# Performance work log

Measured on AMD Instinct MI355X. Metric: run time of the kernel, lower is better.

The kernel has to match this reference:

```python
import jax, jax.numpy as jnp
import numpy as np

B, S = 4096, 256
D = 32  # output_size // 4


def setup_inputs() -> dict:
    key = jax.random.key(0)
    ks = jax.random.split(key, 32)
    # continuous features
    cont_p = jax.random.normal(ks[0], (B, S, 3), dtype=jnp.float32)
    cont_c = jax.random.normal(ks[1], (B, S, 2), dtype=jnp.float32)
    # categorical features, per-column vocab sizes from Embedding tables
    vocabs_p = [2, 2, 2, 11, 34]
    cat_p = jnp.stack([
        jax.random.randint(ks[2 + i], (B, S), 0, v, dtype=jnp.int32)
        for i, v in enumerate(vocabs_p)], axis=2)
    vocabs_c = [19, 31]
    cat_c = jnp.stack([
        jax.random.randint(ks[7 + i], (B, S), 0, v, dtype=jnp.int32)
        for i, v in enumerate(vocabs_c)], axis=2)
    lengths = jax.random.randint(ks[9], (B,), 1, S + 1, dtype=jnp.int32)

    def lin(k, fan_in, fan_out):
        bound = 1.0 / np.sqrt(fan_in)
        kw, kb = jax.random.split(k)
        w = jax.random.uniform(kw, (fan_in, fan_out), jnp.float32, -bound, bound)
        b = jax.random.uniform(kb, (fan_out,), jnp.float32, -bound, bound)
        return w, b

    w_p1, b_p1 = lin(ks[10], 3, D)
    w_p2, b_p2 = lin(ks[11], D, D)
    w_c1, b_c1 = lin(ks[12], 2, D)
    w_c2, b_c2 = lin(ks[13], D, D)
    emb_gender = jax.random.normal(ks[14], (2, D), dtype=jnp.float32)
    emb_korean = jax.random.normal(ks[15], (2, D), dtype=jnp.float32)
    emb_primary = jax.random.normal(ks[16], (2, D), dtype=jnp.float32)
    emb_job = jax.random.normal(ks[17], (11, D), dtype=jnp.float32)
    emb_rep = jax.random.normal(ks[18], (34, D), dtype=jnp.float32)
    emb_place = jax.random.normal(ks[19], (19, D), dtype=jnp.float32)
    emb_add = jax.random.normal(ks[20], (31, D), dtype=jnp.float32)
    w_fc1, b_fc1 = lin(ks[21], 128, 64)
    w_fc2, b_fc2 = lin(ks[22], 64, 2)

    return dict(cont_p=cont_p, cont_c=cont_c, cat_p=cat_p, cat_c=cat_c,
                lengths=lengths,
                w_p1=w_p1, b_p1=b_p1, w_p2=w_p2, b_p2=b_p2,
                w_c1=w_c1, b_c1=b_c1, w_c2=w_c2, b_c2=b_c2,
                emb_gender=emb_gender, emb_korean=emb_korean,
                emb_primary=emb_primary, emb_job=emb_job, emb_rep=emb_rep,
                emb_place=emb_place, emb_add=emb_add,
                w_fc1=w_fc1, b_fc1=b_fc1, w_fc2=w_fc2, b_fc2=b_fc2)


def reference(cont_p, cont_c, cat_p, cat_c, lengths,
              w_p1, b_p1, w_p2, b_p2, w_c1, b_c1, w_c2, b_c2,
              emb_gender, emb_korean, emb_primary, emb_job, emb_rep,
              emb_place, emb_add, w_fc1, b_fc1, w_fc2, b_fc2):
    # small per-token MLPs on continuous features -> [B,S,D]
    hp = jax.nn.relu(cont_p @ w_p1 + b_p1) @ w_p2 + b_p2
    hc = jax.nn.relu(cont_c @ w_c1 + b_c1) @ w_c2 + b_c2
    # multi-table embedding lookups, averaged per group -> [B,S,D]
    ep = (emb_gender[cat_p[:, :, 0]] + emb_korean[cat_p[:, :, 1]] +
          emb_primary[cat_p[:, :, 2]] + emb_job[cat_p[:, :, 3]] +
          emb_rep[cat_p[:, :, 4]]) / 5.0
    ec = (emb_place[cat_c[:, :, 0]] + emb_add[cat_c[:, :, 1]]) / 2.0
    # concat order matches torch: (cat_p, cat_c, cont_p, cont_c) -> [B,S,128]
    x = jnp.concatenate([ep, ec, hp, hc], axis=2)
    # ragged mean pool over first lengths[i] positions (masked segment mean)
    mask = (jnp.arange(x.shape[1])[None, :] < lengths[:, None])
    pooled = jnp.sum(x * mask[:, :, None], axis=1) / lengths[:, None].astype(x.dtype)
    # head: relu(fc1) -> relu(fc2); dropout p=0.0 is identity
    h = jax.nn.relu(pooled @ w_fc1 + b_fc1)
    return jax.nn.relu(h @ w_fc2 + b_fc2)
```

## Files before the change

### kernel.cpp

```cpp
#include <hip/hip_runtime.h>


#define BDIM 64

__device__ __forceinline__ float wave_sum64(float v) {
    #pragma unroll
    for (int d = 32; d; d >>= 1) v += __shfl_xor(v, d);
    return v;
}

__device__ __forceinline__ float transpose_reduce32(const float a[32], int lane) {
    float x16[16];
    {
        const bool s = (lane & 16) != 0;
        #pragma unroll
        for (int i = 0; i < 16; ++i) {
            float keep = s ? a[16 + i] : a[i];
            float send = s ? a[i] : a[16 + i];
            x16[i] = keep + __shfl_xor(send, 16);
        }
    }
    float x8[8];
    {
        const bool s = (lane & 8) != 0;
        #pragma unroll
        for (int i = 0; i < 8; ++i) {
            float keep = s ? x16[8 + i] : x16[i];
            float send = s ? x16[i] : x16[8 + i];
            x8[i] = keep + __shfl_xor(send, 8);
        }
    }
    float x4[4];
    {
        const bool s = (lane & 4) != 0;
        #pragma unroll
        for (int i = 0; i < 4; ++i) {
            float keep = s ? x8[4 + i] : x8[i];
            float send = s ? x8[i] : x8[4 + i];
            x4[i] = keep + __shfl_xor(send, 4);
        }
    }
    float x2[2];
    {
        const bool s = (lane & 2) != 0;
        #pragma unroll
        for (int i = 0; i < 2; ++i) {
            float keep = s ? x2[0] * 0.f + x4[2 + i] : x4[i];
            (void)keep;
            float k2 = s ? x4[2 + i] : x4[i];
            float send = s ? x4[i] : x4[2 + i];
            x2[i] = k2 + __shfl_xor(send, 2);
        }
    }
    float v;
    {
        const bool s = (lane & 1) != 0;
        float keep = s ? x2[1] : x2[0];
        float send = s ? x2[0] : x2[1];
        v = keep + __shfl_xor(send, 1);
    }
    v += __shfl_xor(v, 32);
    return v;
}

__global__ __launch_bounds__(BDIM, 4)
void mlpreg_kernel(const float* __restrict__ cont_p,
                   const float* __restrict__ cont_c,
                   const int* __restrict__ cat_p,
                   const int* __restrict__ cat_c,
                   const int* __restrict__ lengths,
                   const float* __restrict__ w_p1, const float* __restrict__ b_p1,
                   const float* __restrict__ w_p2, const float* __restrict__ b_p2,
                   const float* __restrict__ w_c1, const float* __restrict__ b_c1,
                   const float* __restrict__ w_c2, const float* __restrict__ b_c2,
                   const float* __restrict__ emb_g,  const float* __restrict__ emb_k,
                   const float* __restrict__ emb_pr, const float* __restrict__ emb_j,
                   const float* __restrict__ emb_r,  const float* __restrict__ emb_pl,
                   const float* __restrict__ emb_a,
                   const float* __restrict__ w_fc1, const float* __restrict__ b_fc1,
                   const float* __restrict__ w_fc2, const float* __restrict__ b_fc2,
                   float* __restrict__ out)
{
    constexpr int S = 256;
    __shared__ int   hist[96];
    __shared__ float sPacc[64];
    __shared__ __align__(16) float sPool[128];

    const int lane = threadIdx.x;
    const int b    = blockIdx.x;
    int L = lengths[b];
    L = (L < 1) ? 1 : (L > S ? S : L);
    const float Lf = (float)L, invL = 1.0f / Lf;

    hist[lane] = 0;
    if (lane < 32) hist[64 + lane] = 0;

    const int ch = lane & 31, h = lane >> 5;
    const float* gp = cont_p + (size_t)b * (S * 3);
    const float* gc = cont_c + (size_t)b * (S * 2);
    const int*   kp = cat_p  + (size_t)b * (S * 5);
    const int*   kc = cat_c  + (size_t)b * (S * 2);

    const int t0 = lane, t1 = 64 + lane;
    const int i0 = (t0 < L) ? t0 : (L - 1);
    const int i1 = (t1 < L) ? t1 : (L - 1);
    const float m0 = (t0 < L) ? 1.f : 0.f;
    const float m1 = (t1 < L) ? 1.f : 0.f;
    float a00 = gp[3 * i0], a01 = gp[3 * i0 + 1], a02 = gp[3 * i0 + 2];
    float2 e0 = *(const float2*)&gc[2 * i0];
    float a10 = gp[3 * i1], a11 = gp[3 * i1 + 1], a12 = gp[3 * i1 + 2];
    float2 e1 = *(const float2*)&gc[2 * i1];

    int pk = 0;
    #pragma unroll
    for (int blk = 0; blk < 4; ++blk) {
        if (L > blk * 64) {
            int t = blk * 64 + lane;
            if (t < L) {
                int v0 = kp[5 * t], v1 = kp[5 * t + 1], v2 = kp[5 * t + 2],
                    v3 = kp[5 * t + 3], v4 = kp[5 * t + 4];
                int2 q = *(const int2*)&kc[2 * t];
                pk += v0 + (v1 << 10) + (v2 << 20);
                atomicAdd(&hist[v3], 1);
                atomicAdd(&hist[11 + v4], 1);
                atomicAdd(&hist[46 + q.x], 1);
                atomicAdd(&hist[65 + q.y], 1);
            }
        }
    }
    #pragma unroll
    for (int d = 32; d; d >>= 1) pk += __shfl_xor(pk, d);
    const float sg = (float)(pk & 1023), sk = (float)((pk >> 10) & 1023),
                sp = (float)(pk >> 20);

    float AP[32], AC[32];
    #pragma unroll
    for (int j = 0; j < 32; ++j) {
        float vp = fmaf(a00, w_p1[j], fmaf(a01, w_p1[32 + j], fmaf(a02, w_p1[64 + j], b_p1[j])));
        AP[j] = m0 * fmaxf(vp, 0.f);
        float vc = fmaf(e0.x, w_c1[j], fmaf(e0.y, w_c1[32 + j], b_c1[j]));
        AC[j] = m0 * fmaxf(vc, 0.f);
    }
    if (L > 64) {
        #pragma unroll
        for (int j = 0; j < 32; ++j) {
            float vp = fmaf(a10, w_p1[j], fmaf(a11, w_p1[32 + j], fmaf(a12, w_p1[64 + j], b_p1[j])));
            AP[j] = fmaf(m1, fmaxf(vp, 0.f), AP[j]);
            float vc = fmaf(e1.x, w_c1[j], fmaf(e1.y, w_c1[32 + j], b_c1[j]));
            AC[j] = fmaf(m1, fmaxf(vc, 0.f), AC[j]);
        }
    }
    if (L > 128) {
        int t = 128 + lane;
        int ti = (t < L) ? t : (L - 1);
        float m = (t < L) ? 1.f : 0.f;
        float c0 = gp[3 * ti], c1 = gp[3 * ti + 1], c2 = gp[3 * ti + 2];
        float2 dd = *(const float2*)&gc[2 * ti];
        #pragma unroll
        for (int j = 0; j < 32; ++j) {
            float vp = fmaf(c0, w_p1[j], fmaf(c1, w_p1[32 + j], fmaf(c2, w_p1[64 + j], b_p1[j])));
            AP[j] = fmaf(m, fmaxf(vp, 0.f), AP[j]);
            float vc = fmaf(dd.x, w_c1[j], fmaf(dd.y, w_c1[32 + j], b_c1[j]));
            AC[j] = fmaf(m, fmaxf(vc, 0.f), AC[j]);
        }
    }
    if (L > 192) {
        int t = 192 + lane;
        int ti = (t < L) ? t : (L - 1);
        float m = (t < L) ? 1.f : 0.f;
        float c0 = gp[3 * ti], c1 = gp[3 * ti + 1], c2 = gp[3 * ti + 2];
        float2 dd = *(const float2*)&gc[2 * ti];
        #pragma unroll
        for (int j = 0; j < 32; ++j) {
            float vp = fmaf(c0, w_p1[j], fmaf(c1, w_p1[32 + j], fmaf(c2, w_p1[64 + j], b_p1[j])));
            AP[j] = fmaf(m, fmaxf(vp, 0.f), AP[j]);
            float vc = fmaf(dd.x, w_c1[j], fmaf(dd.y, w_c1[32 + j], b_c1[j]));
            AC[j] = fmaf(m, fmaxf(vc, 0.f), AC[j]);
        }
    }

    float paccP = transpose_reduce32(AP, lane);
    float paccC = transpose_reduce32(AC, lane);
    if (lane < 32) {
        sPacc[ch]      = paccP * invL;
        sPacc[32 + ch] = paccC * invL;
    }
    __syncthreads();

    float vp0 = h ? 0.f : b_p2[ch];
    #pragma unroll
    for (int i = 0; i < 16; ++i) {
        int k = h * 16 + i;
        vp0 = fmaf(sPacc[k], w_p2[k * 32 + ch], vp0);
    }
    vp0 += __shfl_down(vp0, 32);
    float vc0 = h ? 0.f : b_c2[ch];
    #pragma unroll
    for (int i = 0; i < 16; ++i) {
        int k = h * 16 + i;
        vc0 = fmaf(sPacc[32 + k], w_c2[k * 32 + ch], vc0);
    }
    vc0 += __shfl_down(vc0, 32);

    float ep = 0.f;
    if (h == 0) {
        ep  = fmaf(Lf - sg, emb_g[ch],  sg * emb_g[32 + ch]);
        ep += fmaf(Lf - sk, emb_k[ch],  sk * emb_k[32 + ch]);
        ep += fmaf(Lf - sp, emb_pr[ch], sp * emb_pr[32 + ch]);
    }
    #pragma unroll
    for (int i = 0; i < 23; ++i) {
        int bb = 2 * i + h;
        int cnt = hist[bb];
        int br = (bb < 44) ? bb : 44;
        const float* tp = (bb < 11) ? (emb_j + bb * 32) : (emb_r + (br - 11) * 32);
        ep = fmaf((float)cnt, tp[ch], ep);
    }
    ep += __shfl_down(ep, 32);
    float ec = 0.f;
    #pragma unroll
    for (int i = 0; i < 25; ++i) {
        int bb = 46 + 2 * i + h;
        int cnt = hist[bb];
        const float* tp = (bb < 65) ? (emb_pl + (bb - 46) * 32) : (emb_a + (bb - 65) * 32);
        ec = fmaf((float)cnt, tp[ch], ec);
    }
    ec += __shfl_down(ec, 32);

    if (lane < 32) {
        sPool[ch]      = ep * (invL * 0.2f);
        sPool[32 + ch] = ec * (invL * 0.5f);
        sPool[64 + ch] = vp0;
        sPool[96 + ch] = vc0;
    }
    __syncthreads();

    float q0 = b_fc1[lane], q1 = 0.f, q2 = 0.f, q3 = 0.f;
    #pragma unroll
    for (int k4 = 0; k4 < 32; ++k4) {
        float4 x = *(const float4*)&sPool[4 * k4];
        q0 = fmaf(x.x, w_fc1[(size_t)(4 * k4 + 0) * 64 + lane], q0);
        q1 = fmaf(x.y, w_fc1[(size_t)(4 * k4 + 1) * 64 + lane], q1);
        q2 = fmaf(x.z, w_fc1[(size_t)(4 * k4 + 2) * 64 + lane], q2);
        q3 = fmaf(x.w, w_fc1[(size_t)(4 * k4 + 3) * 64 + lane], q3);
    }
    float hv = fmaxf((q0 + q1) + (q2 + q3), 0.f);

    float2 wf = *(const float2*)&w_fc2[2 * lane];
    float p0 = wave_sum64(hv * wf.x);
    float p1 = wave_sum64(hv * wf.y);
    if (lane == 0) {
        float2 o2;
        o2.x = fmaxf(p0 + b_fc2[0], 0.f);
        o2.y = fmaxf(p1 + b_fc2[1], 0.f);
        *(float2*)&out[(size_t)b * 2] = o2;
    }
}

extern "C" void kernel_launch(void* const* d_in, const int* in_sizes, int n_in,
                              void* d_out, int out_size, void* d_ws, size_t ws_size,
                              hipStream_t stream) {
    const float* cont_p = (const float*)d_in[0];
    const float* cont_c = (const float*)d_in[1];
    const int*   cat_p  = (const int*)d_in[2];
    const int*   cat_c  = (const int*)d_in[3];
    const int*   lens   = (const int*)d_in[4];
    const float* w_p1   = (const float*)d_in[5];
    const float* b_p1   = (const float*)d_in[6];
    const float* w_p2   = (const float*)d_in[7];
    const float* b_p2   = (const float*)d_in[8];
    const float* w_c1   = (const float*)d_in[9];
    const float* b_c1   = (const float*)d_in[10];
    const float* w_c2   = (const float*)d_in[11];
    const float* b_c2   = (const float*)d_in[12];
    const float* emb_g  = (const float*)d_in[13];
    const float* emb_k  = (const float*)d_in[14];
    const float* emb_pr = (const float*)d_in[15];
    const float* emb_j  = (const float*)d_in[16];
    const float* emb_r  = (const float*)d_in[17];
    const float* emb_pl = (const float*)d_in[18];
    const float* emb_a  = (const float*)d_in[19];
    const float* w_fc1  = (const float*)d_in[20];
    const float* b_fc1  = (const float*)d_in[21];
    const float* w_fc2  = (const float*)d_in[22];
    const float* b_fc2  = (const float*)d_in[23];
    float* out = (float*)d_out;

    hipLaunchKernelGGL(mlpreg_kernel, dim3(4096), dim3(BDIM), 0, stream,
                       cont_p, cont_c, cat_p, cat_c, lens,
                       w_p1, b_p1, w_p2, b_p2, w_c1, b_c1, w_c2, b_c2,
                       emb_g, emb_k, emb_pr, emb_j, emb_r, emb_pl, emb_a,
                       w_fc1, b_fc1, w_fc2, b_fc2, out);
}
```

Baseline: 162.4 us.

## Stage token features in LDS and loop over tokens with per-lane output channels

Continuous token features are first copied with coalesced loads into a padded shared-memory tile. Each lane then owns one hidden channel (P or C branch) and loops over all valid tokens, reading them as LDS broadcasts. This replaces the per-lane 32-wide register arrays and the transpose-reduce shuffle tree. Work now scales with L and removes the register pressure, but it adds a serial loop of up to 256 iterations per lane and an extra barrier.

```diff
diff --git a/kernel.cpp b/kernel.cpp
--- a/kernel.cpp
+++ b/kernel.cpp
@@ -6,60 +6,6 @@
 __device__ __forceinline__ float wave_sum64(float v) {
     #pragma unroll
     for (int d = 32; d; d >>= 1) v += __shfl_xor(v, d);
-    return v;
-}
-
-__device__ __forceinline__ float transpose_reduce32(const float a[32], int lane) {
-    float x16[16];
-    {
-        const bool s = (lane & 16) != 0;
-        #pragma unroll
-        for (int i = 0; i < 16; ++i) {
-            float keep = s ? a[16 + i] : a[i];
-            float send = s ? a[i] : a[16 + i];
-            x16[i] = keep + __shfl_xor(send, 16);
-        }
-    }
-    float x8[8];
-    {
-        const bool s = (lane & 8) != 0;
-        #pragma unroll
-        for (int i = 0; i < 8; ++i) {
-            float keep = s ? x16[8 + i] : x16[i];
-            float send = s ? x16[i] : x16[8 + i];
-            x8[i] = keep + __shfl_xor(send, 8);
-        }
-    }
-    float x4[4];
-    {
-        const bool s = (lane & 4) != 0;
-        #pragma unroll
-        for (int i = 0; i < 4; ++i) {
-            float keep = s ? x8[4 + i] : x8[i];
-            float send = s ? x8[i] : x8[4 + i];
-            x4[i] = keep + __shfl_xor(send, 4);
-        }
-    }
-    float x2[2];
-    {
-        const bool s = (lane & 2) != 0;
-        #pragma unroll
-        for (int i = 0; i < 2; ++i) {
-            float keep = s ? x2[0] * 0.f + x4[2 + i] : x4[i];
-            (void)keep;
-            float k2 = s ? x4[2 + i] : x4[i];
-            float send = s ? x4[i] : x4[2 + i];
-            x2[i] = k2 + __shfl_xor(send, 2);
-        }
-    }
-    float v;
-    {
-        const bool s = (lane & 1) != 0;
-        float keep = s ? x2[1] : x2[0];
-        float send = s ? x2[0] : x2[1];
-        v = keep + __shfl_xor(send, 1);
-    }
-    v += __shfl_xor(v, 32);
     return v;
 }
 
@@ -82,6 +28,7 @@
                    float* __restrict__ out)
 {
     constexpr int S = 256;
+    __shared__ __align__(16) float sTok[S * 8];
     __shared__ int   hist[96];
     __shared__ float sPacc[64];
     __shared__ __align__(16) float sPool[128];
@@ -101,15 +48,19 @@
     const int*   kp = cat_p  + (size_t)b * (S * 5);
     const int*   kc = cat_c  + (size_t)b * (S * 2);
 
-    const int t0 = lane, t1 = 64 + lane;
-    const int i0 = (t0 < L) ? t0 : (L - 1);
-    const int i1 = (t1 < L) ? t1 : (L - 1);
-    const float m0 = (t0 < L) ? 1.f : 0.f;
-    const float m1 = (t1 < L) ? 1.f : 0.f;
-    float a00 = gp[3 * i0], a01 = gp[3 * i0 + 1], a02 = gp[3 * i0 + 2];
-    float2 e0 = *(const float2*)&gc[2 * i0];
-    float a10 = gp[3 * i1], a11 = gp[3 * i1 + 1], a12 = gp[3 * i1 + 2];
-    float2 e1 = *(const float2*)&gc[2 * i1];
+    const float w0 = h ? w_c1[ch]      : w_p1[ch];
+    const float w1 = h ? w_c1[32 + ch] : w_p1[32 + ch];
+    const float w2 = h ? 0.f           : w_p1[64 + ch];
+    const float bb = h ? b_c1[ch]      : b_p1[ch];
+
+    for (int i = lane; i < 3 * L; i += BDIM) {
+        int t = i / 3, r = i - 3 * t;
+        sTok[t * 8 + r] = gp[i];
+    }
+    for (int i = lane; i < 2 * L; i += BDIM) {
+        int t = i >> 1, r = i & 1;
+        sTok[t * 8 + 4 + r] = gc[i];
+    }
 
     int pk = 0;
     #pragma unroll
@@ -133,58 +84,22 @@
     const float sg = (float)(pk & 1023), sk = (float)((pk >> 10) & 1023),
                 sp = (float)(pk >> 20);
 
-    float AP[32], AC[32];
-    #pragma unroll
-    for (int j = 0; j < 32; ++j) {
-        float vp = fmaf(a00, w_p1[j], fmaf(a01, w_p1[32 + j], fmaf(a02, w_p1[64 + j], b_p1[j])));
-        AP[j] = m0 * fmaxf(vp, 0.f);
-        float vc = fmaf(e0.x, w_c1[j], fmaf(e0.y, w_c1[32 + j], b_c1[j]));
-        AC[j] = m0 * fmaxf(vc, 0.f);
-    }
-    if (L > 64) {
-        #pragma unroll
-        for (int j = 0; j < 32; ++j) {
-            float vp = fmaf(a10, w_p1[j], fmaf(a11, w_p1[32 + j], fmaf(a12, w_p1[64 + j], b_p1[j])));
-            AP[j] = fmaf(m1, fmaxf(vp, 0.f), AP[j]);
-            float vc = fmaf(e1.x, w_c1[j], fmaf(e1.y, w_c1[32 + j], b_c1[j]));
-            AC[j] = fmaf(m1, fmaxf(vc, 0.f), AC[j]);
-        }
-    }
-    if (L > 128) {
-        int t = 128 + lane;
-        int ti = (t < L) ? t : (L - 1);
-        float m = (t < L) ? 1.f : 0.f;
-        float c0 = gp[3 * ti], c1 = gp[3 * ti + 1], c2 = gp[3 * ti + 2];
-        float2 dd = *(const float2*)&gc[2 * ti];
-        #pragma unroll
-        for (int j = 0; j < 32; ++j) {
-            float vp = fmaf(c0, w_p1[j], fmaf(c1, w_p1[32 + j], fmaf(c2, w_p1[64 + j], b_p1[j])));
-            AP[j] = fmaf(m, fmaxf(vp, 0.f), AP[j]);
-            float vc = fmaf(dd.x, w_c1[j], fmaf(dd.y, w_c1[32 + j], b_c1[j]));
-            AC[j] = fmaf(m, fmaxf(vc, 0.f), AC[j]);
-        }
-    }
-    if (L > 192) {
-        int t = 192 + lane;
-        int ti = (t < L) ? t : (L - 1);
-        float m = (t < L) ? 1.f : 0.f;
-        float c0 = gp[3 * ti], c1 = gp[3 * ti + 1], c2 = gp[3 * ti + 2];
-        float2 dd = *(const float2*)&gc[2 * ti];
-        #pragma unroll
-        for (int j = 0; j < 32; ++j) {
-            float vp = fmaf(c0, w_p1[j], fmaf(c1, w_p1[32 + j], fmaf(c2, w_p1[64 + j], b_p1[j])));
-            AP[j] = fmaf(m, fmaxf(vp, 0.f), AP[j]);
-            float vc = fmaf(dd.x, w_c1[j], fmaf(dd.y, w_c1[32 + j], b_c1[j]));
-            AC[j] = fmaf(m, fmaxf(vc, 0.f), AC[j]);
-        }
-    }
-
-    float paccP = transpose_reduce32(AP, lane);
-    float paccC = transpose_reduce32(AC, lane);
-    if (lane < 32) {
-        sPacc[ch]      = paccP * invL;
-        sPacc[32 + ch] = paccC * invL;
-    }
+    __syncthreads();
+
+    const int off = h << 2;
+    float acc0 = 0.f, acc1 = 0.f;
+    int t = 0;
+    for (; t + 1 < L; t += 2) {
+        float4 va = *(const float4*)&sTok[t * 8 + off];
+        float4 vb = *(const float4*)&sTok[(t + 1) * 8 + off];
+        acc0 += fmaxf(fmaf(va.x, w0, fmaf(va.y, w1, fmaf(va.z, w2, bb))), 0.f);
+        acc1 += fmaxf(fmaf(vb.x, w0, fmaf(vb.y, w1, fmaf(vb.z, w2, bb))), 0.f);
+    }
+    if (t < L) {
+        float4 va = *(const float4*)&sTok[t * 8 + off];
+        acc0 += fmaxf(fmaf(va.x, w0, fmaf(va.y, w1, fmaf(va.z, w2, bb))), 0.f);
+    }
+    sPacc[lane] = (acc0 + acc1) * invL;
     __syncthreads();
 
     float vp0 = h ? 0.f : b_p2[ch];
@@ -210,19 +125,19 @@
     }
     #pragma unroll
     for (int i = 0; i < 23; ++i) {
-        int bb = 2 * i + h;
-        int cnt = hist[bb];
-        int br = (bb < 44) ? bb : 44;
-        const float* tp = (bb < 11) ? (emb_j + bb * 32) : (emb_r + (br - 11) * 32);
+        int bb2 = 2 * i + h;
+        int cnt = hist[bb2];
+        int br = (bb2 < 44) ? bb2 : 44;
+        const float* tp = (bb2 < 11) ? (emb_j + bb2 * 32) : (emb_r + (br - 11) * 32);
         ep = fmaf((float)cnt, tp[ch], ep);
     }
     ep += __shfl_down(ep, 32);
     float ec = 0.f;
     #pragma unroll
     for (int i = 0; i < 25; ++i) {
-        int bb = 46 + 2 * i + h;
-        int cnt = hist[bb];
-        const float* tp = (bb < 65) ? (emb_pl + (bb - 46) * 32) : (emb_a + (bb - 65) * 32);
+        int bb2 = 46 + 2 * i + h;
+        int cnt = hist[bb2];
+        const float* tp = (bb2 < 65) ? (emb_pl + (bb2 - 46) * 32) : (emb_a + (bb2 - 65) * 32);
         ec = fmaf((float)cnt, tp[ch], ec);
     }
     ec += __shfl_down(ec, 32);
```

New measurement: 146.5 us. 1.11x faster.
